# Performance work log

Hardware: AMD Instinct MI355X
Metric: run time of the kernel (lower is better)

The kernel has to match this reference:

```python
import jax, jax.numpy as jnp
import numpy as np

BN_EPS = 1e-5


def _gcn_norm(edge_index, n):
    # PyG gcn_norm with add_self_loops=True: deg counts in-degree incl. self loop
    loops = jnp.arange(n, dtype=edge_index.dtype)
    src = jnp.concatenate([edge_index[0], loops])
    dst = jnp.concatenate([edge_index[1], loops])
    deg = jax.ops.segment_sum(jnp.ones(src.shape[0], jnp.float32), dst, num_segments=n)
    dinv = jnp.where(deg > 0, jax.lax.rsqrt(jnp.maximum(deg, 1.0)), 0.0)
    norm = dinv[src] * dinv[dst]  # [E + N]
    return src, dst, norm


def _gcn_conv(x, src, dst, norm, W, b, n):
    h = x @ W                      # dense transform first (fewer FLOPs: d_out gather)
    msgs = h[src] * norm[:, None]  # [E+N, d_out] gathered, degree-normalized
    return jax.ops.segment_sum(msgs, dst, num_segments=n) + b


def _bn_relu(x, gamma, beta):
    # BatchNorm1d in training mode: biased batch stats over node dim
    mu = x.mean(axis=0)
    var = x.var(axis=0)
    return jax.nn.relu(gamma * (x - mu) * jax.lax.rsqrt(var + BN_EPS) + beta)


def setup_inputs() -> dict:
    key = jax.random.key(0)
    ks = jax.random.split(key, 8)
    N, E, D_IN, H1, H2, D_OUT = 50000, 500000, 128, 256, 512, 128
    x = jax.random.normal(ks[0], (N, D_IN), jnp.float32)
    edge_index = jax.random.randint(ks[1], (2, E), 0, N, jnp.int64)
    def lin(k, fan_in, fan_out):
        bound = 1.0 / np.sqrt(fan_in)
        kw, kb = jax.random.split(k)
        W = jax.random.uniform(kw, (fan_in, fan_out), jnp.float32, -bound, bound)
        b = jax.random.uniform(kb, (fan_out,), jnp.float32, -bound, bound)
        return W, b
    W1, b1 = lin(ks[2], D_IN, H1)
    W2, b2 = lin(ks[3], H1, H2)
    Wl, bl = lin(ks[4], H2, D_OUT)
    return {
        "x": x, "edge_index": edge_index,
        "W1": W1, "b1": b1, "gamma1": jnp.ones((H1,), jnp.float32), "beta1": jnp.zeros((H1,), jnp.float32),
        "W2": W2, "b2": b2, "gamma2": jnp.ones((H2,), jnp.float32), "beta2": jnp.zeros((H2,), jnp.float32),
        "Wl": Wl, "bl": bl,
    }


def reference(x, edge_index, W1, b1, gamma1, beta1, W2, b2, gamma2, beta2, Wl, bl):
    n = x.shape[0]
    src, dst, norm = _gcn_norm(edge_index, n)
    h = _bn_relu(_gcn_conv(x, src, dst, norm, W1, b1, n), gamma1, beta1)
    h = _bn_relu(_gcn_conv(h, src, dst, norm, W2, b2, n), gamma2, beta2)
    return h @ Wl + bl
```

## Files before the change

kernel.cpp:

```cpp
#include <hip/hip_runtime.h>
#include <cstdint>
#include <cstddef>

typedef __bf16 bf16;
typedef bf16 bf16x2 __attribute__((ext_vector_type(2)));
typedef bf16 bf16x4 __attribute__((ext_vector_type(4)));
typedef bf16 bf16x8 __attribute__((ext_vector_type(8)));
typedef float f32x4 __attribute__((ext_vector_type(4)));

__global__ void k_init(int* __restrict__ deg, int* __restrict__ cur,
                       float* __restrict__ sums1, float* __restrict__ sums2, int N) {
  int i = blockIdx.x * 256 + threadIdx.x;
  if (i < N) { deg[i] = 1; cur[i] = 0; }
  if (i < 512)  sums1[i] = 0.f;
  if (i < 1024) sums2[i] = 0.f;
}

__global__ void k_count(const int* __restrict__ ei, int* __restrict__ deg, int E) {
  int e = blockIdx.x * 256 + threadIdx.x;
  if (e < E) atomicAdd(&deg[ei[E + e]], 1);
}

__global__ __launch_bounds__(256) void k_scan1(const int* __restrict__ deg,
                                               int* __restrict__ bsum, int N) {
  int t = threadIdx.x;
  int i = blockIdx.x * 256 + t;
  int v = (i < N) ? deg[i] - 1 : 0;
#pragma unroll
  for (int off = 32; off > 0; off >>= 1) v += __shfl_down(v, off, 64);
  __shared__ int red[4];
  if ((t & 63) == 0) red[t >> 6] = v;
  __syncthreads();
  if (t == 0) bsum[blockIdx.x] = red[0] + red[1] + red[2] + red[3];
}

__global__ __launch_bounds__(256) void k_scan2(const int* __restrict__ bsum,
                                               int* __restrict__ bpre, int B) {
  __shared__ int s[256];
  int t = threadIdx.x;
  int v = (t < B) ? bsum[t] : 0;
  s[t] = v;
  __syncthreads();
  for (int off = 1; off < 256; off <<= 1) {
    int add = (t >= off) ? s[t - off] : 0;
    __syncthreads();
    s[t] += add;
    __syncthreads();
  }
  if (t < B) bpre[t] = s[t] - v;
}

__global__ __launch_bounds__(256) void k_scan3(const int* __restrict__ deg,
                                               const int* __restrict__ bpre,
                                               int* __restrict__ roff,
                                               float* __restrict__ dinv, int N) {
  __shared__ int s[256];
  int t = threadIdx.x;
  int i = blockIdx.x * 256 + t;
  int d = (i < N) ? deg[i] : 1;
  int v = d - 1;
  if (i >= N) v = 0;
  s[t] = v;
  __syncthreads();
  for (int off = 1; off < 256; off <<= 1) {
    int add = (t >= off) ? s[t - off] : 0;
    __syncthreads();
    s[t] += add;
    __syncthreads();
  }
  if (i < N) {
    int base = bpre[blockIdx.x];
    roff[i] = base + s[t] - v;
    dinv[i] = rsqrtf((float)d);
    if (i == N - 1) roff[N] = base + s[t];
  }
}

__global__ void k_scatter(const int* __restrict__ ei, const int* __restrict__ roff,
                          int* __restrict__ cur, int* __restrict__ csr, int E) {
  int e = blockIdx.x * 256 + threadIdx.x;
  if (e >= E) return;
  int d = ei[E + e];
  int p = atomicAdd(&cur[d], 1);
  csr[roff[d] + p] = ei[e];
}

__global__ void k_cvt_x(const float* __restrict__ x, bf16* __restrict__ xb, size_t total) {
  size_t base = ((size_t)blockIdx.x * 256 + threadIdx.x) * 4;
  if (base >= total) return;
  const float4 v = *(const float4*)(x + base);
  bf16x4 o;
  o[0] = (bf16)v.x; o[1] = (bf16)v.y; o[2] = (bf16)v.z; o[3] = (bf16)v.w;
  *(bf16x4*)(xb + base) = o;
}

__global__ void k_cvt_w(const float* __restrict__ W1, const float* __restrict__ W2,
                        const float* __restrict__ Wl, bf16* __restrict__ w1t,
                        bf16* __restrict__ w2t, bf16* __restrict__ wlt) {
  int i = blockIdx.x * 256 + threadIdx.x;
  if (i < 32768) {
    int n = i >> 7, k = i & 127;
    w1t[i] = (bf16)W1[(size_t)k * 256 + n];
  } else if (i < 163840) {
    int j = i - 32768;
    int n = j >> 8, k = j & 255;
    w2t[j] = (bf16)W2[(size_t)k * 512 + n];
  } else {
    int j = i - 163840;
    int n = j >> 9, k = j & 511;
    wlt[j] = (bf16)Wl[(size_t)k * 128 + n];
  }
}

template<int K, int NOUT, bool FINAL>
__global__ __launch_bounds__(256) void k_gemm(const bf16* __restrict__ A,
                                              const bf16* __restrict__ Bt,
                                              bf16* __restrict__ outB,
                                              float* __restrict__ outF,
                                              const float* __restrict__ bias,
                                              float* __restrict__ sums,
                                              int Mreal) {
  constexpr int MT  = FINAL ? 64 : 128;
  constexpr int RPW = MT / 32;
  __shared__ uint4 lA[2][MT * 4];
  __shared__ uint4 lB[2][512];
  const int tid = threadIdx.x;
  const int wv = tid >> 6, lane = tid & 63;
  const int q = lane >> 4, mr = lane & 15;
  const int m0 = blockIdx.x * MT;
  const int n0 = blockIdx.y * 128;
  const int rw = (wv >> 1) * (MT / 2), cw = (wv & 1) * 64;

  const int r0 = tid >> 2, j0 = tid & 3;
  const bf16* gA0 = A + (size_t)(m0 + (MT == 64 ? r0 : r0)) * K + j0 * 8;
  const bf16* gA1 = A + (size_t)(m0 + 64 + r0) * K + j0 * 8;
  const bf16* gB0 = Bt + (size_t)(n0 + r0) * K + j0 * 8;
  const bf16* gB1 = Bt + (size_t)(n0 + 64 + r0) * K + j0 * 8;
  const int swz = j0 << 1;
  const int slA0 = j0 * MT + (r0 ^ swz);
  const int slA1 = j0 * MT + ((r0 + 64) ^ swz);
  const int slB0 = j0 * 128 + (r0 ^ swz);
  const int slB1 = j0 * 128 + ((r0 + 64) ^ swz);

  f32x4 acc[RPW][4];
#pragma unroll
  for (int r = 0; r < RPW; ++r)
#pragma unroll
    for (int c = 0; c < 4; ++c) acc[r][c] = (f32x4){0.f, 0.f, 0.f, 0.f};

  uint4 pA0 = *(const uint4*)(gA0);
  uint4 pA1, pB1;
  if constexpr (MT == 128) pA1 = *(const uint4*)(gA1);
  uint4 pB0 = *(const uint4*)(gB0);
  pB1 = *(const uint4*)(gB1);

  const int qs = q << 1;
  int buf = 0;
  for (int k0 = 0; k0 < K; k0 += 32, buf ^= 1) {
    uint4 nA0 = pA0, nA1 = pA1, nB0 = pB0, nB1 = pB1;
    if (k0 + 32 < K) {
      nA0 = *(const uint4*)(gA0 + k0 + 32);
      if constexpr (MT == 128) nA1 = *(const uint4*)(gA1 + k0 + 32);
      nB0 = *(const uint4*)(gB0 + k0 + 32);
      nB1 = *(const uint4*)(gB1 + k0 + 32);
    }
    lA[buf][slA0] = pA0;
    if constexpr (MT == 128) lA[buf][slA1] = pA1;
    lB[buf][slB0] = pB0;
    lB[buf][slB1] = pB1;
    __syncthreads();
    bf16x8 af[RPW], bfr[4];
#pragma unroll
    for (int r = 0; r < RPW; ++r)
      af[r] = ((const bf16x8*)lA[buf])[q * MT + ((rw + r * 16 + mr) ^ qs)];
#pragma unroll
    for (int c = 0; c < 4; ++c)
      bfr[c] = ((const bf16x8*)lB[buf])[q * 128 + ((cw + c * 16 + mr) ^ qs)];
#pragma unroll
    for (int r = 0; r < RPW; ++r)
#pragma unroll
      for (int c = 0; c < 4; ++c)
        acc[r][c] = __builtin_amdgcn_mfma_f32_16x16x32_bf16(af[r], bfr[c], acc[r][c], 0, 0, 0);
    pA0 = nA0; pA1 = nA1; pB0 = nB0; pB1 = nB1;
  }

#pragma unroll
  for (int c = 0; c < 4; ++c) {
    const int col = n0 + cw + c * 16 + mr;
    float s0 = 0.f, s1 = 0.f;
#pragma unroll
    for (int r = 0; r < RPW; ++r) {
#pragma unroll
      for (int i = 0; i < 4; ++i) {
        int row = m0 + rw + r * 16 + q * 4 + i;
        float v = acc[r][c][i];
        if (FINAL) {
          if (row < Mreal) outF[(size_t)row * NOUT + col] = v + bias[col];
        } else {
          outB[(size_t)row * NOUT + col] = (bf16)v;
          if (row < Mreal) { s0 += v; s1 += v * v; }
        }
      }
    }
    if (!FINAL) {
      s0 += __shfl_xor(s0, 16, 64); s0 += __shfl_xor(s0, 32, 64);
      s1 += __shfl_xor(s1, 16, 64); s1 += __shfl_xor(s1, 32, 64);
      if (q == 0) { atomicAdd(&sums[col], s0); atomicAdd(&sums[NOUT + col], s1); }
    }
  }
}

template<int C, bool BN>
__global__ __launch_bounds__(256) void k_agg(const bf16* __restrict__ h,
                                             bf16* __restrict__ g,
                                             const int* __restrict__ csr,
                                             const int* __restrict__ roff,
                                             const float* __restrict__ dinv,
                                             const float* __restrict__ scale,
                                             const float* __restrict__ shift,
                                             int N) {
  constexpr int VPL = C / 64;
  const int lane = threadIdx.x & 63;
  const int v = (int)(((unsigned)blockIdx.x * 256 + threadIdx.x) >> 6);
  if (v >= N) return;
  float sc[VPL], sh[VPL];
  if constexpr (BN) {
#pragma unroll
    for (int u = 0; u < VPL; ++u) { sc[u] = scale[lane * VPL + u]; sh[u] = shift[lane * VPL + u]; }
  }
  const float dv = dinv[v];
  float acc[VPL];
#pragma unroll
  for (int u = 0; u < VPL; ++u) acc[u] = 0.f;

  auto accum = [&](int src, float w) {
    const bf16* hr = h + (size_t)src * C + lane * VPL;
    float vals[VPL];
    if constexpr (VPL == 2) {
      bf16x2 t = *(const bf16x2*)hr;
      vals[0] = (float)t[0]; vals[1] = (float)t[1];
    } else {
      bf16x4 t = *(const bf16x4*)hr;
#pragma unroll
      for (int u = 0; u < 4; ++u) vals[u] = (float)t[u];
    }
#pragma unroll
    for (int u = 0; u < VPL; ++u) {
      float xx = vals[u];
      if constexpr (BN) xx = fmaxf(0.f, xx * sc[u] + sh[u]);
      acc[u] += w * xx;
    }
  };

  accum(v, dv);
  const int beg = roff[v], end = roff[v + 1];
  for (int base = beg; base < end; base += 64) {
    int cnt = min(64, end - base);
    int s = 0; float w = 0.f;
    if (lane < cnt) { s = csr[base + lane]; w = dinv[s]; }
    for (int j = 0; j < cnt; ++j) {
      int sj = __shfl(s, j, 64);
      float wj = __shfl(w, j, 64);
      accum(sj, wj);
    }
  }

  bf16* gv = g + (size_t)v * C + lane * VPL;
  if constexpr (VPL == 2) {
    bf16x2 o;
    o[0] = (bf16)(acc[0] * dv); o[1] = (bf16)(acc[1] * dv);
    *(bf16x2*)gv = o;
  } else {
    bf16x4 o;
#pragma unroll
    for (int u = 0; u < 4; ++u) o[u] = (bf16)(acc[u] * dv);
    *(bf16x4*)gv = o;
  }
}

__global__ void k_bnfinal(const float* __restrict__ sums, const float* __restrict__ gamma,
                          const float* __restrict__ beta, float* __restrict__ scale,
                          float* __restrict__ shift, int C, float invN) {
  int c = blockIdx.x * 256 + threadIdx.x;
  if (c >= C) return;
  float mu = sums[c] * invN;
  float var = sums[C + c] * invN - mu * mu;
  float is = rsqrtf(var + 1e-5f);
  float sc = gamma[c] * is;
  scale[c] = sc;
  shift[c] = beta[c] - mu * sc;
}

template<int C>
__global__ void k_bnapply(bf16* __restrict__ g, const float* __restrict__ scale,
                          const float* __restrict__ shift, size_t total) {
  size_t base = ((size_t)blockIdx.x * 256 + threadIdx.x) * 8;
  if (base >= total) return;
  int col = (int)(base & (size_t)(C - 1));
  bf16x8 t = *(const bf16x8*)(g + base);
  bf16x8 o;
#pragma unroll
  for (int j = 0; j < 8; ++j)
    o[j] = (bf16)fmaxf(0.f, (float)t[j] * scale[col + j] + shift[col + j]);
  *(bf16x8*)(g + base) = o;
}

extern "C" void kernel_launch(void* const* d_in, const int* in_sizes, int n_in,
                              void* d_out, int out_size, void* d_ws, size_t ws_size,
                              hipStream_t stream) {
  const float* x   = (const float*)d_in[0];
  const int*   ei  = (const int*)d_in[1];
  const float* W1  = (const float*)d_in[2];
  const float* g1  = (const float*)d_in[4];
  const float* be1 = (const float*)d_in[5];
  const float* W2  = (const float*)d_in[6];
  const float* g2  = (const float*)d_in[8];
  const float* be2 = (const float*)d_in[9];
  const float* Wl  = (const float*)d_in[10];
  const float* bl  = (const float*)d_in[11];
  float* out = (float*)d_out;

  const int N  = in_sizes[0] / 128;
  const int E  = in_sizes[1] / 2;
  const int Mp = ((N + 127) / 128) * 128;
  const int NB = (N + 255) / 256;

  char* p = (char*)d_ws;
  auto carve = [&](size_t bytes) { void* r = (void*)p; p += (bytes + 255) & ~(size_t)255; return r; };
  int*   deg   = (int*)carve(sizeof(int) * N);
  int*   cur   = (int*)carve(sizeof(int) * N);
  int*   roff  = (int*)carve(sizeof(int) * (N + 1));
  int*   csr   = (int*)carve(sizeof(int) * E);
  int*   bsum  = (int*)carve(sizeof(int) * 256);
  int*   bpre  = (int*)carve(sizeof(int) * 256);
  float* dinv  = (float*)carve(sizeof(float) * N);
  float* sums1 = (float*)carve(sizeof(float) * 512);
  float* sums2 = (float*)carve(sizeof(float) * 1024);
  float* sc1   = (float*)carve(sizeof(float) * 256);
  float* sh1   = (float*)carve(sizeof(float) * 256);
  float* sc2   = (float*)carve(sizeof(float) * 512);
  float* sh2   = (float*)carve(sizeof(float) * 512);
  bf16*  w1t   = (bf16*)carve(sizeof(bf16) * 256 * 128);
  bf16*  w2t   = (bf16*)carve(sizeof(bf16) * 512 * 256);
  bf16*  wlt   = (bf16*)carve(sizeof(bf16) * 128 * 512);
  bf16*  xb    = (bf16*)carve(sizeof(bf16) * (size_t)Mp * 128);
  bf16*  ax1   = (bf16*)carve(sizeof(bf16) * (size_t)Mp * 128);
  bf16*  t1    = (bf16*)carve(sizeof(bf16) * (size_t)Mp * 256);
  bf16*  ax2   = (bf16*)carve(sizeof(bf16) * (size_t)Mp * 256);
  bf16*  t2    = (bf16*)carve(sizeof(bf16) * (size_t)Mp * 512);
  (void)n_in; (void)out_size; (void)ws_size;

  const int gE = (E + 255) / 256;
  k_init<<<NB, 256, 0, stream>>>(deg, cur, sums1, sums2, N);
  k_count<<<gE, 256, 0, stream>>>(ei, deg, E);
  k_scan1<<<NB, 256, 0, stream>>>(deg, bsum, N);
  k_scan2<<<1, 256, 0, stream>>>(bsum, bpre, NB);
  k_scan3<<<NB, 256, 0, stream>>>(deg, bpre, roff, dinv, N);
  k_scatter<<<gE, 256, 0, stream>>>(ei, roff, cur, csr, E);

  k_cvt_x<<<(int)(((size_t)N * 128 / 4 + 255) / 256), 256, 0, stream>>>(x, xb, (size_t)N * 128);
  k_cvt_w<<<896, 256, 0, stream>>>(W1, W2, Wl, w1t, w2t, wlt);

  const int gAgg = (N + 3) / 4;
  k_agg<128, false><<<gAgg, 256, 0, stream>>>(xb, ax1, csr, roff, dinv, nullptr, nullptr, N);
  k_gemm<128, 256, false><<<dim3(Mp / 128, 2), 256, 0, stream>>>(ax1, w1t, t1, nullptr, nullptr, sums1, N);
  k_bnfinal<<<1, 256, 0, stream>>>(sums1, g1, be1, sc1, sh1, 256, 1.f / (float)N);

  k_agg<256, true><<<gAgg, 256, 0, stream>>>(t1, ax2, csr, roff, dinv, sc1, sh1, N);
  k_gemm<256, 512, false><<<dim3(Mp / 128, 4), 256, 0, stream>>>(ax2, w2t, t2, nullptr, nullptr, sums2, N);
  k_bnfinal<<<2, 256, 0, stream>>>(sums2, g2, be2, sc2, sh2, 512, 1.f / (float)N);
  k_bnapply<512><<<(int)(((size_t)Mp * 512 / 8 + 255) / 256), 256, 0, stream>>>(t2, sc2, sh2, (size_t)Mp * 512);

  k_gemm<512, 128, true><<<dim3(Mp / 64, 1), 256, 0, stream>>>(t2, wlt, nullptr, out, bl, nullptr, N);
}
```

Baseline: 380.3 us.

## Use direct global-to-LDS loads in GEMM, stage epilogue through LDS, replace stat atomics

The GEMM kernel now loads tiles with global_load_lds into a double-buffered LDS region, in place of register-staged loads followed by LDS stores. The epilogue goes through LDS so rows are written as coalesced 16-byte vectors. BatchNorm statistics are written as per-block partial sums and reduced in a reworked bnfinal kernel, which replaces global float atomics and the zero-init. The grid is transposed so blockIdx.x indexes N-tiles, and launch bounds request 4 blocks per CU. The cost is extra LDS traffic and syncs in the epilogue, plus a partials buffer.

New measurement: 415.2 us. +9.2%, slower.

```diff
diff --git a/kernel.cpp b/kernel.cpp
--- a/kernel.cpp
+++ b/kernel.cpp
@@ -8,12 +8,14 @@
 typedef bf16 bf16x8 __attribute__((ext_vector_type(8)));
 typedef float f32x4 __attribute__((ext_vector_type(4)));
 
-__global__ void k_init(int* __restrict__ deg, int* __restrict__ cur,
-                       float* __restrict__ sums1, float* __restrict__ sums2, int N) {
+__device__ __forceinline__ void gll16(const void* g, void* l) {
+  __builtin_amdgcn_global_load_lds((__attribute__((address_space(1))) void*)g,
+                                   (__attribute__((address_space(3))) void*)l, 16, 0, 0);
+}
+
+__global__ void k_init(int* __restrict__ deg, int* __restrict__ cur, int N) {
   int i = blockIdx.x * 256 + threadIdx.x;
   if (i < N) { deg[i] = 1; cur[i] = 0; }
-  if (i < 512)  sums1[i] = 0.f;
-  if (i < 1024) sums2[i] = 0.f;
 }
 
 __global__ void k_count(const int* __restrict__ ei, int* __restrict__ deg, int E) {
@@ -113,34 +115,58 @@
 }
 
 template<int K, int NOUT, bool FINAL>
-__global__ __launch_bounds__(256) void k_gemm(const bf16* __restrict__ A,
-                                              const bf16* __restrict__ Bt,
-                                              bf16* __restrict__ outB,
-                                              float* __restrict__ outF,
-                                              const float* __restrict__ bias,
-                                              float* __restrict__ sums,
-                                              int Mreal) {
-  constexpr int MT  = FINAL ? 64 : 128;
-  constexpr int RPW = MT / 32;
-  __shared__ uint4 lA[2][MT * 4];
-  __shared__ uint4 lB[2][512];
+__global__ __launch_bounds__(256, 4) void k_gemm(const bf16* __restrict__ A,
+                                                 const bf16* __restrict__ Bt,
+                                                 bf16* __restrict__ outB,
+                                                 float* __restrict__ outF,
+                                                 const float* __restrict__ bias,
+                                                 float* __restrict__ part,
+                                                 int Mreal) {
+  constexpr int MT    = FINAL ? 64 : 128;
+  constexpr int RPW   = MT / 32;
+  constexpr int NSTEP = K / 32;
+  constexpr int LMT   = FINAL ? 6 : 7;
+  constexpr int SB    = MT * 4 + 512;
+  constexpr int NAI   = (MT * 4) / 256;
+  __shared__ uint4 lds[2 * SB];
+  __shared__ float sstm[512];
+
   const int tid = threadIdx.x;
-  const int wv = tid >> 6, lane = tid & 63;
+  const int wv = tid >> 6;
+  const int lane = tid & 63;
   const int q = lane >> 4, mr = lane & 15;
-  const int m0 = blockIdx.x * MT;
-  const int n0 = blockIdx.y * 128;
+  const int m0 = blockIdx.y * MT;
+  const int n0 = blockIdx.x * 128;
   const int rw = (wv >> 1) * (MT / 2), cw = (wv & 1) * 64;
-
-  const int r0 = tid >> 2, j0 = tid & 3;
-  const bf16* gA0 = A + (size_t)(m0 + (MT == 64 ? r0 : r0)) * K + j0 * 8;
-  const bf16* gA1 = A + (size_t)(m0 + 64 + r0) * K + j0 * 8;
-  const bf16* gB0 = Bt + (size_t)(n0 + r0) * K + j0 * 8;
-  const bf16* gB1 = Bt + (size_t)(n0 + 64 + r0) * K + j0 * 8;
-  const int swz = j0 << 1;
-  const int slA0 = j0 * MT + (r0 ^ swz);
-  const int slA1 = j0 * MT + ((r0 + 64) ^ swz);
-  const int slB0 = j0 * 128 + (r0 ^ swz);
-  const int slB1 = j0 * 128 + ((r0 + 64) ^ swz);
+  const int qs = q << 1;
+  const int wslot = wv << 6;
+
+  const bf16* srcA[NAI];
+#pragma unroll
+  for (int p = 0; p < NAI; ++p) {
+    int slot = p * 256 + tid;
+    int jj = slot >> LMT, sl = slot & (MT - 1);
+    int row = sl ^ (jj << 1);
+    srcA[p] = A + (size_t)(m0 + row) * K + jj * 8;
+  }
+  const bf16* srcB[2];
+#pragma unroll
+  for (int p = 0; p < 2; ++p) {
+    int slot = p * 256 + tid;
+    int jj = slot >> 7, sl = slot & 127;
+    int row = sl ^ (jj << 1);
+    srcB[p] = Bt + (size_t)(n0 + row) * K + jj * 8;
+  }
+
+  auto issue = [&](int t) {
+    uint4* bb = lds + (t & 1) * SB;
+#pragma unroll
+    for (int p = 0; p < NAI; ++p)
+      gll16(srcA[p] + t * 32, bb + p * 256 + wslot);
+#pragma unroll
+    for (int p = 0; p < 2; ++p)
+      gll16(srcB[p] + t * 32, bb + MT * 4 + p * 256 + wslot);
+  };
 
   f32x4 acc[RPW][4];
 #pragma unroll
@@ -148,64 +174,94 @@
 #pragma unroll
     for (int c = 0; c < 4; ++c) acc[r][c] = (f32x4){0.f, 0.f, 0.f, 0.f};
 
-  uint4 pA0 = *(const uint4*)(gA0);
-  uint4 pA1, pB1;
-  if constexpr (MT == 128) pA1 = *(const uint4*)(gA1);
-  uint4 pB0 = *(const uint4*)(gB0);
-  pB1 = *(const uint4*)(gB1);
-
-  const int qs = q << 1;
-  int buf = 0;
-  for (int k0 = 0; k0 < K; k0 += 32, buf ^= 1) {
-    uint4 nA0 = pA0, nA1 = pA1, nB0 = pB0, nB1 = pB1;
-    if (k0 + 32 < K) {
-      nA0 = *(const uint4*)(gA0 + k0 + 32);
-      if constexpr (MT == 128) nA1 = *(const uint4*)(gA1 + k0 + 32);
-      nB0 = *(const uint4*)(gB0 + k0 + 32);
-      nB1 = *(const uint4*)(gB1 + k0 + 32);
-    }
-    lA[buf][slA0] = pA0;
-    if constexpr (MT == 128) lA[buf][slA1] = pA1;
-    lB[buf][slB0] = pB0;
-    lB[buf][slB1] = pB1;
-    __syncthreads();
-    bf16x8 af[RPW], bfr[4];
-#pragma unroll
-    for (int r = 0; r < RPW; ++r)
-      af[r] = ((const bf16x8*)lA[buf])[q * MT + ((rw + r * 16 + mr) ^ qs)];
+  issue(0);
+  __syncthreads();
+
+#pragma unroll
+  for (int t = 0; t < NSTEP; ++t) {
+    if (t + 1 < NSTEP) issue(t + 1);
+
+    const uint4* bb = lds + (t & 1) * SB;
+    const bf16x8* bA = (const bf16x8*)bb;
+    const bf16x8* bB = (const bf16x8*)(bb + MT * 4);
+    bf16x8 bfr[4];
 #pragma unroll
     for (int c = 0; c < 4; ++c)
-      bfr[c] = ((const bf16x8*)lB[buf])[q * 128 + ((cw + c * 16 + mr) ^ qs)];
-#pragma unroll
-    for (int r = 0; r < RPW; ++r)
+      bfr[c] = bB[q * 128 + ((cw + c * 16 + mr) ^ qs)];
+#pragma unroll
+    for (int r = 0; r < RPW; ++r) {
+      bf16x8 af = bA[q * MT + ((rw + r * 16 + mr) ^ qs)];
 #pragma unroll
       for (int c = 0; c < 4; ++c)
-        acc[r][c] = __builtin_amdgcn_mfma_f32_16x16x32_bf16(af[r], bfr[c], acc[r][c], 0, 0, 0);
-    pA0 = nA0; pA1 = nA1; pB0 = nB0; pB1 = nB1;
-  }
-
-#pragma unroll
-  for (int c = 0; c < 4; ++c) {
-    const int col = n0 + cw + c * 16 + mr;
-    float s0 = 0.f, s1 = 0.f;
-#pragma unroll
-    for (int r = 0; r < RPW; ++r) {
-#pragma unroll
-      for (int i = 0; i < 4; ++i) {
-        int row = m0 + rw + r * 16 + q * 4 + i;
-        float v = acc[r][c][i];
-        if (FINAL) {
-          if (row < Mreal) outF[(size_t)row * NOUT + col] = v + bias[col];
-        } else {
-          outB[(size_t)row * NOUT + col] = (bf16)v;
-          if (row < Mreal) { s0 += v; s1 += v * v; }
+        acc[r][c] = __builtin_amdgcn_mfma_f32_16x16x32_bf16(af, bfr[c], acc[r][c], 0, 0, 0);
+    }
+    __syncthreads();
+  }
+
+  if constexpr (!FINAL) {
+    bf16* ot = (bf16*)lds;
+#pragma unroll
+    for (int c = 0; c < 4; ++c) {
+      float s0 = 0.f, s1 = 0.f;
+#pragma unroll
+      for (int r = 0; r < RPW; ++r) {
+#pragma unroll
+        for (int i = 0; i < 4; ++i) {
+          int rl = rw + r * 16 + q * 4 + i;
+          int cl = cw + c * 16 + mr;
+          float v = acc[r][c][i];
+          ot[rl * 128 + (cl ^ (((rl >> 2) & 3) << 4))] = (bf16)v;
+          if (m0 + rl < Mreal) { s0 += v; s1 += v * v; }
         }
       }
-    }
-    if (!FINAL) {
       s0 += __shfl_xor(s0, 16, 64); s0 += __shfl_xor(s0, 32, 64);
       s1 += __shfl_xor(s1, 16, 64); s1 += __shfl_xor(s1, 32, 64);
-      if (q == 0) { atomicAdd(&sums[col], s0); atomicAdd(&sums[NOUT + col], s1); }
+      if (q == 0) {
+        sstm[wv * 64 + c * 16 + mr] = s0;
+        sstm[256 + wv * 64 + c * 16 + mr] = s1;
+      }
+    }
+    __syncthreads();
+    {
+      int ssel = tid >> 7, cl = tid & 127;
+      int hi = cl >> 6, lo = cl & 63;
+      float v = sstm[ssel * 256 + hi * 64 + lo] + sstm[ssel * 256 + (hi + 2) * 64 + lo];
+      part[((size_t)ssel * gridDim.y + blockIdx.y) * NOUT + n0 + cl] = v;
+    }
+#pragma unroll
+    for (int p = 0; p < 8; ++p) {
+      int rl = p * 16 + (tid >> 4), c8 = tid & 15;
+      uint4 v = *(const uint4*)(ot + rl * 128 + ((c8 * 8) ^ (((rl >> 2) & 3) << 4)));
+      *(uint4*)(outB + (size_t)(m0 + rl) * NOUT + n0 + c8 * 8) = v;
+    }
+  } else {
+    float* otf = (float*)lds;
+#pragma unroll
+    for (int h = 0; h < 2; ++h) {
+      __syncthreads();
+#pragma unroll
+      for (int c = 0; c < 4; ++c)
+#pragma unroll
+        for (int r = 0; r < RPW; ++r)
+#pragma unroll
+          for (int i = 0; i < 4; ++i) {
+            int rl = rw + r * 16 + q * 4 + i;
+            if ((rl >> 5) != h) continue;
+            int cl = cw + c * 16 + mr;
+            otf[(rl - h * 32) * 128 + (cl ^ (((rl >> 2) & 3) << 4))] = acc[r][c][i];
+          }
+      __syncthreads();
+#pragma unroll
+      for (int p = 0; p < 4; ++p) {
+        int rl = p * 8 + (tid >> 5), c4 = tid & 31;
+        int rg = m0 + h * 32 + rl;
+        if (rg < Mreal) {
+          float4 v = *(const float4*)(otf + rl * 128 + ((c4 * 4) ^ ((((rl + h * 32) >> 2) & 3) << 4)));
+          const float4 bv = *(const float4*)(bias + c4 * 4);
+          v.x += bv.x; v.y += bv.y; v.z += bv.z; v.w += bv.w;
+          *(float4*)(outF + (size_t)rg * 128 + c4 * 4) = v;
+        }
+      }
     }
   }
 }
@@ -278,17 +334,33 @@
   }
 }
 
-__global__ void k_bnfinal(const float* __restrict__ sums, const float* __restrict__ gamma,
-                          const float* __restrict__ beta, float* __restrict__ scale,
-                          float* __restrict__ shift, int C, float invN) {
-  int c = blockIdx.x * 256 + threadIdx.x;
-  if (c >= C) return;
-  float mu = sums[c] * invN;
-  float var = sums[C + c] * invN - mu * mu;
-  float is = rsqrtf(var + 1e-5f);
-  float sc = gamma[c] * is;
-  scale[c] = sc;
-  shift[c] = beta[c] - mu * sc;
+__global__ __launch_bounds__(256) void k_bnfinal(const float* __restrict__ part,
+                                                 const float* __restrict__ gamma,
+                                                 const float* __restrict__ beta,
+                                                 float* __restrict__ scale,
+                                                 float* __restrict__ shift,
+                                                 int C, int GX, float invN) {
+  __shared__ float red[2][4][64];
+  int t = threadIdx.x;
+  int cl = t & 63, seg = t >> 6;
+  int c = blockIdx.x * 64 + cl;
+  float s0 = 0.f, s1 = 0.f;
+  for (int b = seg; b < GX; b += 4) {
+    s0 += part[(size_t)b * C + c];
+    s1 += part[(size_t)(GX + b) * C + c];
+  }
+  red[0][seg][cl] = s0; red[1][seg][cl] = s1;
+  __syncthreads();
+  if (seg == 0) {
+    s0 = red[0][0][cl] + red[0][1][cl] + red[0][2][cl] + red[0][3][cl];
+    s1 = red[1][0][cl] + red[1][1][cl] + red[1][2][cl] + red[1][3][cl];
+    float mu = s0 * invN;
+    float var = s1 * invN - mu * mu;
+    float is = rsqrtf(var + 1e-5f);
+    float scv = gamma[c] * is;
+    scale[c] = scv;
+    shift[c] = beta[c] - mu * scv;
+  }
 }
 
 template<int C>
@@ -324,6 +396,7 @@
   const int E  = in_sizes[1] / 2;
   const int Mp = ((N + 127) / 128) * 128;
   const int NB = (N + 255) / 256;
+  const int GX = Mp / 128;
 
   char* p = (char*)d_ws;
   auto carve = [&](size_t bytes) { void* r = (void*)p; p += (bytes + 255) & ~(size_t)255; return r; };
@@ -334,8 +407,8 @@
   int*   bsum  = (int*)carve(sizeof(int) * 256);
   int*   bpre  = (int*)carve(sizeof(int) * 256);
   float* dinv  = (float*)carve(sizeof(float) * N);
-  float* sums1 = (float*)carve(sizeof(float) * 512);
-  float* sums2 = (float*)carve(sizeof(float) * 1024);
+  float* part1 = (float*)carve(sizeof(float) * 2 * (size_t)GX * 256);
+  float* part2 = (float*)carve(sizeof(float) * 2 * (size_t)GX * 512);
   float* sc1   = (float*)carve(sizeof(float) * 256);
   float* sh1   = (float*)carve(sizeof(float) * 256);
   float* sc2   = (float*)carve(sizeof(float) * 512);
@@ -351,7 +424,7 @@
   (void)n_in; (void)out_size; (void)ws_size;
 
   const int gE = (E + 255) / 256;
-  k_init<<<NB, 256, 0, stream>>>(deg, cur, sums1, sums2, N);
+  k_init<<<NB, 256, 0, stream>>>(deg, cur, N);
   k_count<<<gE, 256, 0, stream>>>(ei, deg, E);
   k_scan1<<<NB, 256, 0, stream>>>(deg, bsum, N);
   k_scan2<<<1, 256, 0, stream>>>(bsum, bpre, NB);
@@ -363,13 +436,13 @@
 
   const int gAgg = (N + 3) / 4;
   k_agg<128, false><<<gAgg, 256, 0, stream>>>(xb, ax1, csr, roff, dinv, nullptr, nullptr, N);
-  k_gemm<128, 256, false><<<dim3(Mp / 128, 2), 256, 0, stream>>>(ax1, w1t, t1, nullptr, nullptr, sums1, N);
-  k_bnfinal<<<1, 256, 0, stream>>>(sums1, g1, be1, sc1, sh1, 256, 1.f / (float)N);
+  k_gemm<128, 256, false><<<dim3(2, GX), 256, 0, stream>>>(ax1, w1t, t1, nullptr, nullptr, part1, N);
+  k_bnfinal<<<4, 256, 0, stream>>>(part1, g1, be1, sc1, sh1, 256, GX, 1.f / (float)N);
 
   k_agg<256, true><<<gAgg, 256, 0, stream>>>(t1, ax2, csr, roff, dinv, sc1, sh1, N);
-  k_gemm<256, 512, false><<<dim3(Mp / 128, 4), 256, 0, stream>>>(ax2, w2t, t2, nullptr, nullptr, sums2, N);
-  k_bnfinal<<<2, 256, 0, stream>>>(sums2, g2, be2, sc2, sh2, 512, 1.f / (float)N);
+  k_gemm<256, 512, false><<<dim3(4, GX), 256, 0, stream>>>(ax2, w2t, t2, nullptr, nullptr, part2, N);
+  k_bnfinal<<<8, 256, 0, stream>>>(part2, g2, be2, sc2, sh2, 512, GX, 1.f / (float)N);
   k_bnapply<512><<<(int)(((size_t)Mp * 512 / 8 + 255) / 256), 256, 0, stream>>>(t2, sc2, sh2, (size_t)Mp * 512);
 
-  k_gemm<512, 128, true><<<dim3(Mp / 64, 1), 256, 0, stream>>>(t2, wlt, nullptr, out, bl, nullptr, N);
-}
+  k_gemm<512, 128, true><<<dim3(1, Mp / 64), 256, 0, stream>>>(t2, wlt, nullptr, out, bl, nullptr, N);
+}
```
